# Optimization experiments

Measured on AMD Instinct MI355X. Metric: run time of the kernel, lower is better.

The kernel has to match this reference:

```python
import jax, jax.numpy as jnp
import numpy as np

D = 1024       # hidden_size
H = 16         # num_heads
DH = D // H    # d_keys = d_values = 64
FF = int(D * 2.0)  # mlp hidden
EPS = 1e-6


def _ln(t):
    # LayerNorm, elementwise_affine=False
    mu = jnp.mean(t, axis=-1, keepdims=True)
    var = jnp.mean((t - mu) ** 2, axis=-1, keepdims=True)
    return (t - mu) * jax.lax.rsqrt(var + EPS)


def setup_inputs() -> dict:
    key = jax.random.key(0)
    ks = jax.random.split(key, 16)
    B, L = 2, 2048
    s = 0.02
    return {
        "x": jax.random.normal(ks[0], (B, L, D), jnp.float32),
        "c": jax.random.normal(ks[1], (B, 1, D), jnp.float32),
        "Wq": jax.random.normal(ks[2], (D, D), jnp.float32) * s,
        "bq": jnp.zeros((D,), jnp.float32),
        "Wk": jax.random.normal(ks[3], (D, D), jnp.float32) * s,
        "bk": jnp.zeros((D,), jnp.float32),
        "Wv": jax.random.normal(ks[4], (D, D), jnp.float32) * s,
        "bv": jnp.zeros((D,), jnp.float32),
        "Wo": jax.random.normal(ks[5], (D, D), jnp.float32) * s,
        "bo": jnp.zeros((D,), jnp.float32),
        "W1": jax.random.normal(ks[6], (D, FF), jnp.float32) * s,
        "b1": jnp.zeros((FF,), jnp.float32),
        "W2": jax.random.normal(ks[7], (FF, D), jnp.float32) * s,
        "b2": jnp.zeros((D,), jnp.float32),
        "Wada": jax.random.normal(ks[8], (D, 6 * D), jnp.float32) * s,
        "bada": jnp.zeros((6 * D,), jnp.float32),
    }


def reference(x, c, Wq, bq, Wk, bk, Wv, bv, Wo, bo, W1, b1, W2, b2, Wada, bada):
    B, L, _ = x.shape
    # adaLN-Zero modulation params (dropout layers act as identity in eval)
    ada = jax.nn.silu(c) @ Wada + bada  # [B,1,6D]
    shift_msa, scale_msa, gate_msa, shift_mlp, scale_mlp, gate_mlp = jnp.split(ada, 6, axis=-1)

    # --- attention branch ---
    h = _ln(x) * (1.0 + scale_msa) + shift_msa
    q = (h @ Wq + bq).reshape(B, L, H, DH)
    k = (h @ Wk + bk).reshape(B, L, H, DH)
    v = (h @ Wv + bv).reshape(B, L, H, DH)
    scale = 1.0 / np.sqrt(DH).astype(np.float32)
    scores = jnp.einsum('blhe,bshe->bhls', q, k)  # full LxL scores, as in source
    A = jax.nn.softmax(scale * scores, axis=-1)
    out = jnp.einsum('bhls,bshd->blhd', A, v)     # [B,L,H,DH]
    # mix=True: transpose(2,1) then view(B,L,-1) -> head/position mixing reshape
    out = jnp.transpose(out, (0, 2, 1, 3)).reshape(B, L, H * DH)
    x = x + gate_msa * (out @ Wo + bo)

    # --- MLP branch (exact GELU: nn.GELU() passed as act_layer) ---
    h2 = _ln(x) * (1.0 + scale_mlp) + shift_mlp
    m = jax.nn.gelu(h2 @ W1 + b1, approximate=False) @ W2 + b2
    return x + gate_mlp * m
```

## Files before the change

### kernel.cpp

```cpp
#include <hip/hip_runtime.h>
#include <hip/hip_bf16.h>

typedef unsigned short ushort_t;
typedef __bf16 bf16x8 __attribute__((ext_vector_type(8)));
typedef float f32x4 __attribute__((ext_vector_type(4)));

typedef unsigned int u32;
typedef u32 __attribute__((address_space(1))) global_u32;
typedef u32 __attribute__((address_space(3))) lds_u32;

#define D_ 1024
#define L_ 2048
#define B_ 2
#define H_ 16
#define DH_ 64
#define FF_ 2048
#define ADA_ 6144
#define BHL_ (B_ * H_ * L_)

#define MFMA __builtin_amdgcn_mfma_f32_16x16x32_bf16

__device__ __forceinline__ ushort_t f2bf(float f) {
    union { float f; u32 u; } v; v.f = f;
    u32 r = v.u + 0x7fffu + ((v.u >> 16) & 1u);
    return (ushort_t)(r >> 16);
}

__device__ __forceinline__ u32 pk_bf16(float a, float b) {
    float2 f; f.x = a; f.y = b;
    __hip_bfloat162 t = __float22bfloat162_rn(f);
    union { __hip_bfloat162 b2; u32 u; } v; v.b2 = t; return v.u;
}

__device__ __forceinline__ void llds16(const ushort_t* src, ushort_t* dst) {
    __builtin_amdgcn_global_load_lds((global_u32*)src, (lds_u32*)dst, 16, 0, 0);
}

__global__ void transpose_w_all(
    const float* __restrict__ Wq, const float* __restrict__ Wk,
    const float* __restrict__ Wv, const float* __restrict__ Wo,
    const float* __restrict__ W1, const float* __restrict__ W2,
    ushort_t* __restrict__ Wqkv, ushort_t* __restrict__ Wo_t,
    ushort_t* __restrict__ W1_t, ushort_t* __restrict__ W2_t) {
    __shared__ float tile[64][65];
    int id = blockIdx.x;
    const float* W; ushort_t* Wt; int K, N, ntx, lid;
    if (id < 1024) {
        int which = id >> 8; lid = id & 255; K = 1024; N = 1024; ntx = 16;
        W  = which == 0 ? Wq : which == 1 ? Wk : which == 2 ? Wv : Wo;
        Wt = which == 3 ? Wo_t : Wqkv + (size_t)which * 1024 * 1024;
    } else if (id < 1536) {
        lid = id - 1024; W = W1; Wt = W1_t; K = 1024; N = 2048; ntx = 32;
    } else {
        lid = id - 1536; W = W2; Wt = W2_t; K = 2048; N = 1024; ntx = 16;
    }
    int n0 = (lid % ntx) * 64, k0 = (lid / ntx) * 64;
    int t = threadIdx.x;
    for (int p = 0; p < 4; ++p) {
        int k = p * 16 + (t >> 4), nn = (t & 15) * 4;
        float4 v = *(const float4*)(W + (size_t)(k0 + k) * N + n0 + nn);
        tile[k][nn] = v.x; tile[k][nn + 1] = v.y; tile[k][nn + 2] = v.z; tile[k][nn + 3] = v.w;
    }
    __syncthreads();
    for (int p = 0; p < 4; ++p) {
        int n = p * 16 + (t >> 4), kk = (t & 15) * 4;
        ushort4 o;
        o.x = f2bf(tile[kk][n]); o.y = f2bf(tile[kk + 1][n]);
        o.z = f2bf(tile[kk + 2][n]); o.w = f2bf(tile[kk + 3][n]);
        *(ushort4*)(Wt + (size_t)(n0 + n) * K + k0 + kk) = o;
    }
}

__global__ void transpose_v(const ushort_t* __restrict__ V, ushort_t* __restrict__ Vt) {
    __shared__ ushort_t tile[64][72];
    int bh = blockIdx.y, l0 = blockIdx.x * 64;
    const ushort_t* Vb = V + ((size_t)bh * L_ + l0) * DH_;
    ushort_t* Vtb = Vt + (size_t)bh * DH_ * L_;
    int t = threadIdx.x;
    for (int p = 0; p < 2; ++p) {
        int i = p * 32 + (t >> 3), d0 = (t & 7) * 8;
        ushort4 v0 = *(const ushort4*)(Vb + (size_t)i * DH_ + d0);
        ushort4 v1 = *(const ushort4*)(Vb + (size_t)i * DH_ + d0 + 4);
        tile[d0 + 0][i] = v0.x; tile[d0 + 1][i] = v0.y; tile[d0 + 2][i] = v0.z; tile[d0 + 3][i] = v0.w;
        tile[d0 + 4][i] = v1.x; tile[d0 + 5][i] = v1.y; tile[d0 + 6][i] = v1.z; tile[d0 + 7][i] = v1.w;
    }
    __syncthreads();
    for (int p = 0; p < 2; ++p) {
        int dh = p * 32 + (t >> 3), j0 = (t & 7) * 8;
        ushort4 o0, o1;
        o0.x = tile[dh][j0 + 0]; o0.y = tile[dh][j0 + 1]; o0.z = tile[dh][j0 + 2]; o0.w = tile[dh][j0 + 3];
        o1.x = tile[dh][j0 + 4]; o1.y = tile[dh][j0 + 5]; o1.z = tile[dh][j0 + 6]; o1.w = tile[dh][j0 + 7];
        *(ushort4*)(Vtb + (size_t)dh * L_ + l0 + j0) = o0;
        *(ushort4*)(Vtb + (size_t)dh * L_ + l0 + j0 + 4) = o1;
    }
}

__global__ void ada_gemv(const float* __restrict__ c, const float* __restrict__ Wada,
                         float* __restrict__ partial) {
    int ks = blockIdx.y;
    int j = blockIdx.x * 256 + threadIdx.x;
    __shared__ float s0[64], s1[64];
    if (threadIdx.x < 64) {
        float v = c[ks * 64 + threadIdx.x];
        s0[threadIdx.x] = v / (1.f + __expf(-v));
        v = c[D_ + ks * 64 + threadIdx.x];
        s1[threadIdx.x] = v / (1.f + __expf(-v));
    }
    __syncthreads();
    float a0 = 0.f, a1 = 0.f;
#pragma unroll 8
    for (int d = 0; d < 64; ++d) {
        float w = Wada[(size_t)(ks * 64 + d) * ADA_ + j];
        a0 = fmaf(s0[d], w, a0);
        a1 = fmaf(s1[d], w, a1);
    }
    partial[(size_t)(ks * 2 + 0) * ADA_ + j] = a0;
    partial[(size_t)(ks * 2 + 1) * ADA_ + j] = a1;
}

__global__ void ada_reduce(const float* __restrict__ partial,
                           const float* __restrict__ bada, float* __restrict__ ada) {
    int j = blockIdx.x * 256 + threadIdx.x;
    float a0 = bada[j], a1 = bada[j];
#pragma unroll
    for (int ks = 0; ks < 16; ++ks) {
        a0 += partial[(size_t)(ks * 2 + 0) * ADA_ + j];
        a1 += partial[(size_t)(ks * 2 + 1) * ADA_ + j];
    }
    ada[j] = a0;
    ada[ADA_ + j] = a1;
}

__global__ void ln_mod(const float* __restrict__ x, const float* __restrict__ ada,
                       int so, int co, ushort_t* __restrict__ out) {
    int row = blockIdx.x;
    int b = row >> 11;
    float4 v = ((const float4*)(x + (size_t)row * D_))[threadIdx.x];
    float sum = v.x + v.y + v.z + v.w;
    float sq = v.x * v.x + v.y * v.y + v.z * v.z + v.w * v.w;
    for (int off = 32; off; off >>= 1) { sum += __shfl_down(sum, off); sq += __shfl_down(sq, off); }
    __shared__ float sa[4], sb[4];
    int wave = threadIdx.x >> 6, lane = threadIdx.x & 63;
    if (lane == 0) { sa[wave] = sum; sb[wave] = sq; }
    __syncthreads();
    sum = sa[0] + sa[1] + sa[2] + sa[3];
    sq = sb[0] + sb[1] + sb[2] + sb[3];
    float mean = sum * (1.f / 1024.f);
    float var = sq * (1.f / 1024.f) - mean * mean;
    float rstd = rsqrtf(var + 1e-6f);
    int d = threadIdx.x * 4;
    const float* shf = ada + (size_t)b * ADA_ + so;
    const float* scf = ada + (size_t)b * ADA_ + co;
    uint2 ov;
    ov.x = pk_bf16((v.x - mean) * rstd * (1.f + scf[d + 0]) + shf[d + 0],
                   (v.y - mean) * rstd * (1.f + scf[d + 1]) + shf[d + 1]);
    ov.y = pk_bf16((v.z - mean) * rstd * (1.f + scf[d + 2]) + shf[d + 2],
                   (v.w - mean) * rstd * (1.f + scf[d + 3]) + shf[d + 3]);
    *(uint2*)(out + (size_t)row * D_ + d) = ov;
}

struct EpiArgs {
    const float* bias0; const float* bias1; const float* bias2;
    ushort_t* o0; ushort_t* o1; ushort_t* o2;
    const float* resid; const float* gate;
    float* fout;
};

template <int EPI>
__device__ __forceinline__ void epi_store(float v, int m, int n, int N, const EpiArgs& e) {
    if (EPI == 0) {
        int which = n >> 10, cc = n & 1023;
        const float* bias = which == 0 ? e.bias0 : which == 1 ? e.bias1 : e.bias2;
        ushort_t* ob = which == 0 ? e.o0 : which == 1 ? e.o1 : e.o2;
        v += bias[cc];
        if (which == 0) v *= 0.18033688f;
        int b = m >> 11, l = m & 2047, h = cc >> 6, dh = cc & 63;
        ob[(((size_t)(b * H_ + h) * L_) + l) * DH_ + dh] = f2bf(v);
    } else if (EPI == 1) {
        v += e.bias0[n];
        v = 0.5f * v * (1.f + erff(v * 0.70710678118f));
        e.o0[(size_t)m * N + n] = f2bf(v);
    } else {
        int b = m >> 11;
        e.fout[(size_t)m * N + n] =
            e.resid[(size_t)m * N + n] + e.gate[(size_t)b * ADA_ + n] * (v + e.bias0[n]);
    }
}

template <int EPI>
__device__ __forceinline__ void st4(const f32x4& cc, int mb, int n, int N, const EpiArgs& e) {
#pragma unroll
    for (int r = 0; r < 4; ++r) epi_store<EPI>(cc[r], mb + r, n, N, e);
}

template <int EPI>
__global__ __launch_bounds__(256, 2) void gemm_bt(
    const ushort_t* __restrict__ A, const ushort_t* __restrict__ Bt,
    int M, int N, int K, EpiArgs e) {
    __shared__ ushort_t As[128 * 64];
    __shared__ ushort_t Bs[128 * 64];
    int m0 = blockIdx.x * 128, n0 = blockIdx.y * 128;
    int tid = threadIdx.x, wave = tid >> 6, lane = tid & 63;
    int quad = lane >> 4, lc = lane & 15;
    int wm = (wave & 1) * 64, wn = (wave >> 1) * 64;
    int srow = lane >> 3, sg = lane & 7;
    int sw = lc & 7;

    const ushort_t* stp[8];
    ushort_t* stl[8];
#pragma unroll
    for (int i = 0; i < 8; ++i) {
        int chunk = wave * 8 + i;
        int c = chunk & 15;
        int row = c * 8 + srow;
        stp[i] = (chunk < 16 ? A + (size_t)(m0 + row) * K
                             : Bt + (size_t)(n0 + row) * K) + (sg ^ srow) * 8;
        stl[i] = (chunk < 16 ? As : Bs) + c * 512 + lane * 8;
    }

    f32x4 c00 = {}, c01 = {}, c02 = {}, c03 = {};
    f32x4 c10 = {}, c11 = {}, c12 = {}, c13 = {};
    f32x4 c20 = {}, c21 = {}, c22 = {}, c23 = {};
    f32x4 c30 = {}, c31 = {}, c32 = {}, c33 = {};

    for (int k0 = 0; k0 < K; k0 += 64) {
#pragma unroll
        for (int i = 0; i < 8; ++i) { llds16(stp[i], stl[i]); stp[i] += 64; }
        __syncthreads();
#pragma unroll
        for (int kk = 0; kk < 2; ++kk) {
            int off = ((kk * 4 + quad) ^ sw) * 8;
            bf16x8 a0 = *(const bf16x8*)&As[(wm +  0 + lc) * 64 + off];
            bf16x8 a1 = *(const bf16x8*)&As[(wm + 16 + lc) * 64 + off];
            bf16x8 a2 = *(const bf16x8*)&As[(wm + 32 + lc) * 64 + off];
            bf16x8 a3 = *(const bf16x8*)&As[(wm + 48 + lc) * 64 + off];
            bf16x8 b0 = *(const bf16x8*)&Bs[(wn +  0 + lc) * 64 + off];
            bf16x8 b1 = *(const bf16x8*)&Bs[(wn + 16 + lc) * 64 + off];
            bf16x8 b2 = *(const bf16x8*)&Bs[(wn + 32 + lc) * 64 + off];
            bf16x8 b3 = *(const bf16x8*)&Bs[(wn + 48 + lc) * 64 + off];
            c00 = MFMA(a0, b0, c00, 0, 0, 0); c01 = MFMA(a0, b1, c01, 0, 0, 0);
            c02 = MFMA(a0, b2, c02, 0, 0, 0); c03 = MFMA(a0, b3, c03, 0, 0, 0);
            c10 = MFMA(a1, b0, c10, 0, 0, 0); c11 = MFMA(a1, b1, c11, 0, 0, 0);
            c12 = MFMA(a1, b2, c12, 0, 0, 0); c13 = MFMA(a1, b3, c13, 0, 0, 0);
            c20 = MFMA(a2, b0, c20, 0, 0, 0); c21 = MFMA(a2, b1, c21, 0, 0, 0);
            c22 = MFMA(a2, b2, c22, 0, 0, 0); c23 = MFMA(a2, b3, c23, 0, 0, 0);
            c30 = MFMA(a3, b0, c30, 0, 0, 0); c31 = MFMA(a3, b1, c31, 0, 0, 0);
            c32 = MFMA(a3, b2, c32, 0, 0, 0); c33 = MFMA(a3, b3, c33, 0, 0, 0);
        }
        __syncthreads();
    }

    int mb = m0 + wm + quad * 4, nb = n0 + wn + lc;
    st4<EPI>(c00, mb +  0, nb +  0, N, e); st4<EPI>(c01, mb +  0, nb + 16, N, e);
    st4<EPI>(c02, mb +  0, nb + 32, N, e); st4<EPI>(c03, mb +  0, nb + 48, N, e);
    st4<EPI>(c10, mb + 16, nb +  0, N, e); st4<EPI>(c11, mb + 16, nb + 16, N, e);
    st4<EPI>(c12, mb + 16, nb + 32, N, e); st4<EPI>(c13, mb + 16, nb + 48, N, e);
    st4<EPI>(c20, mb + 32, nb +  0, N, e); st4<EPI>(c21, mb + 32, nb + 16, N, e);
    st4<EPI>(c22, mb + 32, nb + 32, N, e); st4<EPI>(c23, mb + 32, nb + 48, N, e);
    st4<EPI>(c30, mb + 48, nb +  0, N, e); st4<EPI>(c31, mb + 48, nb + 16, N, e);
    st4<EPI>(c32, mb + 48, nb + 32, N, e); st4<EPI>(c33, mb + 48, nb + 48, N, e);
}

template <int EPI>
__global__ __launch_bounds__(256, 2) void gemm_bt64(
    const ushort_t* __restrict__ A, const ushort_t* __restrict__ Bt,
    int M, int N, int K, EpiArgs e) {
    __shared__ ushort_t As[64 * 64];
    __shared__ ushort_t Bs[128 * 64];
    int m0 = blockIdx.x * 64, n0 = blockIdx.y * 128;
    int tid = threadIdx.x, wave = tid >> 6, lane = tid & 63;
    int quad = lane >> 4, lc = lane & 15;
    int wn = wave * 32;
    int srow = lane >> 3, sg = lane & 7;
    int sw = lc & 7;

    const ushort_t* stp[6];
    ushort_t* stl[6];
#pragma unroll
    for (int i = 0; i < 6; ++i) {
        int chunk = wave * 6 + i;
        if (chunk < 8) {
            int row = chunk * 8 + srow;
            stp[i] = A + (size_t)(m0 + row) * K + (sg ^ srow) * 8;
            stl[i] = &As[chunk * 512 + lane * 8];
        } else {
            int c = chunk - 8;
            int row = c * 8 + srow;
            stp[i] = Bt + (size_t)(n0 + row) * K + (sg ^ srow) * 8;
            stl[i] = &Bs[c * 512 + lane * 8];
        }
    }

    f32x4 c00 = {}, c01 = {};
    f32x4 c10 = {}, c11 = {};
    f32x4 c20 = {}, c21 = {};
    f32x4 c30 = {}, c31 = {};

    for (int k0 = 0; k0 < K; k0 += 64) {
#pragma unroll
        for (int i = 0; i < 6; ++i) { llds16(stp[i], stl[i]); stp[i] += 64; }
        __syncthreads();
#pragma unroll
        for (int kk = 0; kk < 2; ++kk) {
            int off = ((kk * 4 + quad) ^ sw) * 8;
            bf16x8 a0 = *(const bf16x8*)&As[( 0 + lc) * 64 + off];
            bf16x8 a1 = *(const bf16x8*)&As[(16 + lc) * 64 + off];
            bf16x8 a2 = *(const bf16x8*)&As[(32 + lc) * 64 + off];
            bf16x8 a3 = *(const bf16x8*)&As[(48 + lc) * 64 + off];
            bf16x8 b0 = *(const bf16x8*)&Bs[(wn +  0 + lc) * 64 + off];
            bf16x8 b1 = *(const bf16x8*)&Bs[(wn + 16 + lc) * 64 + off];
            c00 = MFMA(a0, b0, c00, 0, 0, 0); c01 = MFMA(a0, b1, c01, 0, 0, 0);
            c10 = MFMA(a1, b0, c10, 0, 0, 0); c11 = MFMA(a1, b1, c11, 0, 0, 0);
            c20 = MFMA(a2, b0, c20, 0, 0, 0); c21 = MFMA(a2, b1, c21, 0, 0, 0);
            c30 = MFMA(a3, b0, c30, 0, 0, 0); c31 = MFMA(a3, b1, c31, 0, 0, 0);
        }
        __syncthreads();
    }

    int mb = m0 + quad * 4, nb = n0 + wn + lc;
    st4<EPI>(c00, mb +  0, nb + 0, N, e); st4<EPI>(c01, mb +  0, nb + 16, N, e);
    st4<EPI>(c10, mb + 16, nb + 0, N, e); st4<EPI>(c11, mb + 16, nb + 16, N, e);
    st4<EPI>(c20, mb + 32, nb + 0, N, e); st4<EPI>(c21, mb + 32, nb + 16, N, e);
    st4<EPI>(c30, mb + 48, nb + 0, N, e); st4<EPI>(c31, mb + 48, nb + 16, N, e);
}

__global__ __launch_bounds__(256, 2) void attn(
    const ushort_t* __restrict__ Q, const ushort_t* __restrict__ Kx,
    const ushort_t* __restrict__ Vt,
    ushort_t* __restrict__ Op0, ushort_t* __restrict__ Op1,
    ushort_t* __restrict__ Op2, ushort_t* __restrict__ Op3,
    float* __restrict__ lsum) {
    __shared__ ushort_t Ks[128 * 64];
    __shared__ ushort_t Vs[64 * 128];
    __shared__ ushort_t Ps[4 * 16 * 128];
    int id = blockIdx.x;
    int bh = ((id & 7) << 2) + ((id >> 3) & 3);
    int quarter = (id >> 5) & 3;
    int qt = id >> 7;
    const ushort_t* Qg = Q + ((size_t)bh * L_ + qt * 128) * DH_;
    const ushort_t* Kg = Kx + (size_t)bh * L_ * DH_;
    const ushort_t* Vg = Vt + (size_t)bh * DH_ * L_;
    int tid = threadIdx.x, wave = tid >> 6, lane = tid & 63;
    int quad = lane >> 4, lc = lane & 15;
    int sw = lc & 7;
    int srow = lane >> 3, sg = lane & 7;

    const ushort_t* stp[8];
    ushort_t* stl[8];
    int stinc;
    if (wave < 2) {
        stinc = 128 * DH_;
#pragma unroll
        for (int i = 0; i < 8; ++i) {
            int chunk = wave * 8 + i;
            int row = chunk * 8 + srow;
            stp[i] = Kg + (size_t)(quarter * 512 + row) * DH_ + (sg ^ srow) * 8;
            stl[i] = &Ks[chunk * 512 + lane * 8];
        }
    } else {
        stinc = 128;
#pragma unroll
        for (int i = 0; i < 8; ++i) {
            int c2 = (wave - 2) * 8 + i;
            int row = c2 * 4 + (lane >> 4);
            int g = (lane & 15) ^ (row & 15);
            stp[i] = Vg + (size_t)row * L_ + quarter * 512 + g * 8;
            stl[i] = &Vs[c2 * 512 + lane * 8];
        }
    }

    const ushort_t* qp = Qg + (size_t)(wave * 32 + lc) * DH_ + quad * 8;
    bf16x8 q00 = *(const bf16x8*)(qp);
    bf16x8 q01 = *(const bf16x8*)(qp + 32);
    bf16x8 q10 = *(const bf16x8*)(qp + 16 * DH_);
    bf16x8 q11 = *(const bf16x8*)(qp + 16 * DH_ + 32);

    f32x4 o00 = {}, o01 = {}, o02 = {}, o03 = {};
    f32x4 o10 = {}, o11 = {}, o12 = {}, o13 = {};
    float lrow0 = 0.f, lrow1 = 0.f;
    ushort_t* Pw = &Ps[wave * 16 * 128];

    for (int t = 0; t < 4; ++t) {
#pragma unroll
        for (int i = 0; i < 8; ++i) { llds16(stp[i], stl[i]); stp[i] += stinc; }
        __syncthreads();

        f32x4 s[2][8];
#pragma unroll
        for (int kk = 0; kk < 2; ++kk) {
            int off = ((kk * 4 + quad) ^ sw) * 8;
            bf16x8 aq0 = kk == 0 ? q00 : q01;
            bf16x8 aq1 = kk == 0 ? q10 : q11;
#pragma unroll
            for (int ni = 0; ni < 8; ++ni) {
                bf16x8 bk = *(const bf16x8*)&Ks[(ni * 16 + lc) * 64 + off];
                if (kk == 0) {
                    f32x4 z = {0.f, 0.f, 0.f, 0.f};
                    s[0][ni] = MFMA(bk, aq0, z, 0, 0, 0);
                    s[1][ni] = MFMA(bk, aq1, z, 0, 0, 0);
                } else {
                    s[0][ni] = MFMA(bk, aq0, s[0][ni], 0, 0, 0);
                    s[1][ni] = MFMA(bk, aq1, s[1][ni], 0, 0, 0);
                }
            }
        }

#pragma unroll
        for (int pi = 0; pi < 2; ++pi) {
            float acc = 0.f;
#pragma unroll
            for (int ni = 0; ni < 8; ++ni) {
                float p0 = __builtin_amdgcn_exp2f(s[pi][ni][0]);
                float p1 = __builtin_amdgcn_exp2f(s[pi][ni][1]);
                float p2 = __builtin_amdgcn_exp2f(s[pi][ni][2]);
                float p3 = __builtin_amdgcn_exp2f(s[pi][ni][3]);
                acc += (p0 + p1) + (p2 + p3);
                uint2 pk; pk.x = pk_bf16(p0, p1); pk.y = pk_bf16(p2, p3);
                int cg = ni * 2 + (quad >> 1);
                *(uint2*)&Pw[lc * 128 + ((cg ^ lc) & 15) * 8 + (quad & 1) * 4] = pk;
            }
            acc += __shfl_xor(acc, 16);
            acc += __shfl_xor(acc, 32);
            if (pi == 0) lrow0 += acc; else lrow1 += acc;

#pragma unroll
            for (int kk = 0; kk < 4; ++kk) {
                int gq = kk * 4 + quad;
                bf16x8 ap  = *(const bf16x8*)&Pw[lc * 128 + ((gq ^ lc) & 15) * 8];
                bf16x8 bv0 = *(const bf16x8*)&Vs[( 0 + lc) * 128 + ((gq ^ lc) * 8)];
                bf16x8 bv1 = *(const bf16x8*)&Vs[(16 + lc) * 128 + ((gq ^ lc) * 8)];
                bf16x8 bv2 = *(const bf16x8*)&Vs[(32 + lc) * 128 + ((gq ^ lc) * 8)];
                bf16x8 bv3 = *(const bf16x8*)&Vs[(48 + lc) * 128 + ((gq ^ lc) * 8)];
                if (pi == 0) {
                    o00 = MFMA(ap, bv0, o00, 0, 0, 0); o01 = MFMA(ap, bv1, o01, 0, 0, 0);
                    o02 = MFMA(ap, bv2, o02, 0, 0, 0); o03 = MFMA(ap, bv3, o03, 0, 0, 0);
                } else {
                    o10 = MFMA(ap, bv0, o10, 0, 0, 0); o11 = MFMA(ap, bv1, o11, 0, 0, 0);
                    o12 = MFMA(ap, bv2, o12, 0, 0, 0); o13 = MFMA(ap, bv3, o13, 0, 0, 0);
                }
            }
        }
        __syncthreads();
    }

    ushort_t* Op = quarter == 0 ? Op0 : quarter == 1 ? Op1 : quarter == 2 ? Op2 : Op3;
#pragma unroll
    for (int pi = 0; pi < 2; ++pi) {
#pragma unroll
        for (int nio = 0; nio < 4; ++nio) {
            const f32x4& ov = pi == 0 ? (nio == 0 ? o00 : nio == 1 ? o01 : nio == 2 ? o02 : o03)
                                      : (nio == 0 ? o10 : nio == 1 ? o11 : nio == 2 ? o12 : o13);
#pragma unroll
            for (int r = 0; r < 4; ++r) {
                int row = qt * 128 + wave * 32 + pi * 16 + quad * 4 + r;
                Op[((size_t)bh * L_ + row) * DH_ + nio * 16 + lc] = f2bf(ov[r]);
            }
        }
    }
    if (quad == 0) {
        int base = qt * 128 + wave * 32;
        lsum[(size_t)quarter * BHL_ + (size_t)bh * L_ + base + lc] = lrow0;
        lsum[(size_t)quarter * BHL_ + (size_t)bh * L_ + base + 16 + lc] = lrow1;
    }
}

__global__ void attn_merge(const ushort_t* __restrict__ Op0,
                           const ushort_t* __restrict__ Op1,
                           const ushort_t* __restrict__ Op2,
                           const ushort_t* __restrict__ Op3,
                           const float* __restrict__ lsum,
                           ushort_t* __restrict__ O) {
    int gid = blockIdx.x * 256 + threadIdx.x;
    int row = gid >> 3, j = gid & 7;
    float inv = 1.f / (lsum[row] + lsum[BHL_ + row] +
                       lsum[2 * BHL_ + row] + lsum[3 * BHL_ + row]);
    bf16x8 v0 = *(const bf16x8*)(Op0 + (size_t)row * DH_ + j * 8);
    bf16x8 v1 = *(const bf16x8*)(Op1 + (size_t)row * DH_ + j * 8);
    bf16x8 v2 = *(const bf16x8*)(Op2 + (size_t)row * DH_ + j * 8);
    bf16x8 v3 = *(const bf16x8*)(Op3 + (size_t)row * DH_ + j * 8);
    uint4 o;
    float r0, r1;
#pragma unroll
    for (int k = 0; k < 4; ++k) {
        r0 = ((float)v0[2 * k] + (float)v1[2 * k] + (float)v2[2 * k] + (float)v3[2 * k]) * inv;
        r1 = ((float)v0[2 * k + 1] + (float)v1[2 * k + 1] + (float)v2[2 * k + 1] + (float)v3[2 * k + 1]) * inv;
        ((u32*)&o)[k] = pk_bf16(r0, r1);
    }
    *(uint4*)(O + (size_t)row * DH_ + j * 8) = o;
}

extern "C" void kernel_launch(void* const* d_in, const int* in_sizes, int n_in,
                              void* d_out, int out_size, void* d_ws, size_t ws_size,
                              hipStream_t stream) {
    (void)in_sizes; (void)n_in; (void)out_size; (void)ws_size;
    const float* x    = (const float*)d_in[0];
    const float* c    = (const float*)d_in[1];
    const float* Wq   = (const float*)d_in[2];
    const float* bq   = (const float*)d_in[3];
    const float* Wk   = (const float*)d_in[4];
    const float* bk   = (const float*)d_in[5];
    const float* Wv   = (const float*)d_in[6];
    const float* bv   = (const float*)d_in[7];
    const float* Wo   = (const float*)d_in[8];
    const float* bo   = (const float*)d_in[9];
    const float* W1   = (const float*)d_in[10];
    const float* b1   = (const float*)d_in[11];
    const float* W2   = (const float*)d_in[12];
    const float* b2   = (const float*)d_in[13];
    const float* Wada = (const float*)d_in[14];
    const float* bada = (const float*)d_in[15];

    char* w = (char*)d_ws;
    float*    ada  = (float*)(w + 0);
    ushort_t* Wqkv = (ushort_t*)(w + 49152);
    ushort_t* Wo_t = (ushort_t*)(w + 6340608);
    ushort_t* W1_t = (ushort_t*)(w + 8437760);
    ushort_t* W2_t = (ushort_t*)(w + 12632064);
    ushort_t* h    = (ushort_t*)(w + 16826368);
    ushort_t* Qb   = (ushort_t*)(w + 25214976);
    ushort_t* Kb   = (ushort_t*)(w + 33603584);
    ushort_t* Vb   = (ushort_t*)(w + 41992192);
    ushort_t* Vtb  = (ushort_t*)(w + 50380800);
    float*    x1   = (float*)(w + 58769408);
    ushort_t* Ob   = Qb;
    ushort_t* m1   = Qb;
    float*    lsb  = (float*)Wqkv;
    float*    adap = (float*)Vtb;
    ushort_t* p2   = (ushort_t*)x1;
    ushort_t* p3   = (ushort_t*)((char*)x1 + 8388608);

    const int M = B_ * L_;

    transpose_w_all<<<2048, 256, 0, stream>>>(Wq, Wk, Wv, Wo, W1, W2,
                                              Wqkv, Wo_t, W1_t, W2_t);

    ada_gemv<<<dim3(24, 16), 256, 0, stream>>>(c, Wada, adap);
    ada_reduce<<<24, 256, 0, stream>>>(adap, bada, ada);
    ln_mod<<<M, 256, 0, stream>>>(x, ada, 0, 1024, h);

    EpiArgs e0 = {bq, bk, bv, Qb, Kb, Vb, nullptr, nullptr, nullptr};
    gemm_bt<0><<<dim3(32, 24), 256, 0, stream>>>(h, Wqkv, M, 3072, D_, e0);

    transpose_v<<<dim3(32, 32), 256, 0, stream>>>(Vb, Vtb);

    attn<<<2048, 256, 0, stream>>>(Qb, Kb, Vtb, Vb, h, p2, p3, lsb);
    attn_merge<<<2048, 256, 0, stream>>>(Vb, h, p2, p3, lsb, Ob);

    EpiArgs e1 = {bo, nullptr, nullptr, nullptr, nullptr, nullptr, x, ada + 2048, x1};
    gemm_bt64<2><<<dim3(64, 8), 256, 0, stream>>>(Ob, Wo_t, M, D_, D_, e1);

    ln_mod<<<M, 256, 0, stream>>>(x1, ada, 3072, 4096, h);

    EpiArgs e2 = {b1, nullptr, nullptr, m1, nullptr, nullptr, nullptr, nullptr, nullptr};
    gemm_bt64<1><<<dim3(64, 16), 256, 0, stream>>>(h, W1_t, M, FF_, D_, e2);

    EpiArgs e3 = {b2, nullptr, nullptr, nullptr, nullptr, nullptr, x1, ada + 5120, (float*)d_out};
    gemm_bt64<2><<<dim3(64, 8), 256, 0, stream>>>(m1, W2_t, M, D_, FF_, e3);
}
```

Baseline: 323.6 us.

## Double-buffer K/V tiles in attention kernel and raise MFMA wave priority

Double-buffers the K and V shared-memory tiles in the attention kernel. The next tile is issued with direct global-to-LDS loads before the current tile is computed, and partial vmcnt waits plus raw barriers hide global latency behind the MFMA work. It also raises wave priority around the MFMA sections with s_setprio. The extra 32 KB of LDS per block may cut occupancy below the requested two blocks per CU, and the hand-written waitcnt counts must match the number of loads in flight.

```diff
diff --git a/kernel.cpp b/kernel.cpp
--- a/kernel.cpp
+++ b/kernel.cpp
@@ -330,8 +330,8 @@
     ushort_t* __restrict__ Op0, ushort_t* __restrict__ Op1,
     ushort_t* __restrict__ Op2, ushort_t* __restrict__ Op3,
     float* __restrict__ lsum) {
-    __shared__ ushort_t Ks[128 * 64];
-    __shared__ ushort_t Vs[64 * 128];
+    __shared__ ushort_t Ks[2][128 * 64];
+    __shared__ ushort_t Vs[2][64 * 128];
     __shared__ ushort_t Ps[4 * 16 * 128];
     int id = blockIdx.x;
     int bh = ((id & 7) << 2) + ((id >> 3) & 3);
@@ -355,7 +355,7 @@
             int chunk = wave * 8 + i;
             int row = chunk * 8 + srow;
             stp[i] = Kg + (size_t)(quarter * 512 + row) * DH_ + (sg ^ srow) * 8;
-            stl[i] = &Ks[chunk * 512 + lane * 8];
+            stl[i] = &Ks[0][chunk * 512 + lane * 8];
         }
     } else {
         stinc = 128;
@@ -365,9 +365,12 @@
             int row = c2 * 4 + (lane >> 4);
             int g = (lane & 15) ^ (row & 15);
             stp[i] = Vg + (size_t)row * L_ + quarter * 512 + g * 8;
-            stl[i] = &Vs[c2 * 512 + lane * 8];
-        }
-    }
+            stl[i] = &Vs[0][c2 * 512 + lane * 8];
+        }
+    }
+
+#pragma unroll
+    for (int i = 0; i < 8; ++i) { llds16(stp[i], stl[i]); stp[i] += stinc; }
 
     const ushort_t* qp = Qg + (size_t)(wave * 32 + lc) * DH_ + quad * 8;
     bf16x8 q00 = *(const bf16x8*)(qp);
@@ -381,11 +384,21 @@
     ushort_t* Pw = &Ps[wave * 16 * 128];
 
     for (int t = 0; t < 4; ++t) {
-#pragma unroll
-        for (int i = 0; i < 8; ++i) { llds16(stp[i], stl[i]); stp[i] += stinc; }
-        __syncthreads();
+        if (t < 3) {
+            int nbuf = (t + 1) & 1;
+#pragma unroll
+            for (int i = 0; i < 8; ++i) { llds16(stp[i], stl[i] + nbuf * 8192); stp[i] += stinc; }
+            asm volatile("s_waitcnt vmcnt(8)" ::: "memory");
+        } else {
+            asm volatile("s_waitcnt vmcnt(0)" ::: "memory");
+        }
+        __builtin_amdgcn_s_barrier();
+        asm volatile("" ::: "memory");
+        const ushort_t* Ksb = &Ks[t & 1][0];
+        const ushort_t* Vsb = &Vs[t & 1][0];
 
         f32x4 s[2][8];
+        __builtin_amdgcn_s_setprio(1);
 #pragma unroll
         for (int kk = 0; kk < 2; ++kk) {
             int off = ((kk * 4 + quad) ^ sw) * 8;
@@ -393,7 +406,7 @@
             bf16x8 aq1 = kk == 0 ? q10 : q11;
 #pragma unroll
             for (int ni = 0; ni < 8; ++ni) {
-                bf16x8 bk = *(const bf16x8*)&Ks[(ni * 16 + lc) * 64 + off];
+                bf16x8 bk = *(const bf16x8*)&Ksb[(ni * 16 + lc) * 64 + off];
                 if (kk == 0) {
                     f32x4 z = {0.f, 0.f, 0.f, 0.f};
                     s[0][ni] = MFMA(bk, aq0, z, 0, 0, 0);
@@ -404,6 +417,7 @@
                 }
             }
         }
+        __builtin_amdgcn_s_setprio(0);
 
 #pragma unroll
         for (int pi = 0; pi < 2; ++pi) {
@@ -423,14 +437,15 @@
             acc += __shfl_xor(acc, 32);
             if (pi == 0) lrow0 += acc; else lrow1 += acc;
 
+            __builtin_amdgcn_s_setprio(1);
 #pragma unroll
             for (int kk = 0; kk < 4; ++kk) {
                 int gq = kk * 4 + quad;
                 bf16x8 ap  = *(const bf16x8*)&Pw[lc * 128 + ((gq ^ lc) & 15) * 8];
-                bf16x8 bv0 = *(const bf16x8*)&Vs[( 0 + lc) * 128 + ((gq ^ lc) * 8)];
-                bf16x8 bv1 = *(const bf16x8*)&Vs[(16 + lc) * 128 + ((gq ^ lc) * 8)];
-                bf16x8 bv2 = *(const bf16x8*)&Vs[(32 + lc) * 128 + ((gq ^ lc) * 8)];
-                bf16x8 bv3 = *(const bf16x8*)&Vs[(48 + lc) * 128 + ((gq ^ lc) * 8)];
+                bf16x8 bv0 = *(const bf16x8*)&Vsb[( 0 + lc) * 128 + ((gq ^ lc) * 8)];
+                bf16x8 bv1 = *(const bf16x8*)&Vsb[(16 + lc) * 128 + ((gq ^ lc) * 8)];
+                bf16x8 bv2 = *(const bf16x8*)&Vsb[(32 + lc) * 128 + ((gq ^ lc) * 8)];
+                bf16x8 bv3 = *(const bf16x8*)&Vsb[(48 + lc) * 128 + ((gq ^ lc) * 8)];
                 if (pi == 0) {
                     o00 = MFMA(ap, bv0, o00, 0, 0, 0); o01 = MFMA(ap, bv1, o01, 0, 0, 0);
                     o02 = MFMA(ap, bv2, o02, 0, 0, 0); o03 = MFMA(ap, bv3, o03, 0, 0, 0);
@@ -439,8 +454,10 @@
                     o12 = MFMA(ap, bv2, o12, 0, 0, 0); o13 = MFMA(ap, bv3, o13, 0, 0, 0);
                 }
             }
-        }
-        __syncthreads();
+            __builtin_amdgcn_s_setprio(0);
+        }
+        asm volatile("" ::: "memory");
+        __builtin_amdgcn_s_barrier();
     }
 
     ushort_t* Op = quarter == 0 ? Op0 : quarter == 1 ? Op1 : quarter == 2 ? Op2 : Op3;
```

Measured after the change: 339.0 us. 4.8% more time.

## Keep softmax probabilities in registers by permuting K rows to match MFMA layout

Applied to the files above, without the earlier changes.

Stops staging the bf16 probability tile through shared memory between the QK and PV MFMAs. K rows are loaded in a permuted order so the QK accumulator layout already matches the A-operand layout the PV MFMA needs, and packed probabilities are assembled directly into MFMA operands. This removes LDS writes and reads plus 16 KB of shared memory per block. In exchange it holds more live registers (the px/py arrays), which could limit occupancy.

```diff
diff --git a/kernel.cpp b/kernel.cpp
--- a/kernel.cpp
+++ b/kernel.cpp
@@ -332,7 +332,6 @@
     float* __restrict__ lsum) {
     __shared__ ushort_t Ks[128 * 64];
     __shared__ ushort_t Vs[64 * 128];
-    __shared__ ushort_t Ps[4 * 16 * 128];
     int id = blockIdx.x;
     int bh = ((id & 7) << 2) + ((id >> 3) & 3);
     int quarter = (id >> 5) & 3;
@@ -353,8 +352,10 @@
 #pragma unroll
         for (int i = 0; i < 8; ++i) {
             int chunk = wave * 8 + i;
-            int row = chunk * 8 + srow;
-            stp[i] = Kg + (size_t)(quarter * 512 + row) * DH_ + (sg ^ srow) * 8;
+            int slot = chunk * 8 + srow;
+            int s5 = slot & 31;
+            int sig = (slot & ~31) + ((s5 & 15) >> 2) * 8 + (s5 & 3) + (s5 >> 4) * 4;
+            stp[i] = Kg + (size_t)(quarter * 512 + sig) * DH_ + (sg ^ srow) * 8;
             stl[i] = &Ks[chunk * 512 + lane * 8];
         }
     } else {
@@ -378,7 +379,6 @@
     f32x4 o00 = {}, o01 = {}, o02 = {}, o03 = {};
     f32x4 o10 = {}, o11 = {}, o12 = {}, o13 = {};
     float lrow0 = 0.f, lrow1 = 0.f;
-    ushort_t* Pw = &Ps[wave * 16 * 128];
 
     for (int t = 0; t < 4; ++t) {
 #pragma unroll
@@ -405,6 +405,7 @@
             }
         }
 
+        u32 px[2][8], py[2][8];
 #pragma unroll
         for (int pi = 0; pi < 2; ++pi) {
             float acc = 0.f;
@@ -415,30 +416,30 @@
                 float p2 = __builtin_amdgcn_exp2f(s[pi][ni][2]);
                 float p3 = __builtin_amdgcn_exp2f(s[pi][ni][3]);
                 acc += (p0 + p1) + (p2 + p3);
-                uint2 pk; pk.x = pk_bf16(p0, p1); pk.y = pk_bf16(p2, p3);
-                int cg = ni * 2 + (quad >> 1);
-                *(uint2*)&Pw[lc * 128 + ((cg ^ lc) & 15) * 8 + (quad & 1) * 4] = pk;
+                px[pi][ni] = pk_bf16(p0, p1);
+                py[pi][ni] = pk_bf16(p2, p3);
             }
             acc += __shfl_xor(acc, 16);
             acc += __shfl_xor(acc, 32);
             if (pi == 0) lrow0 += acc; else lrow1 += acc;
-
-#pragma unroll
-            for (int kk = 0; kk < 4; ++kk) {
-                int gq = kk * 4 + quad;
-                bf16x8 ap  = *(const bf16x8*)&Pw[lc * 128 + ((gq ^ lc) & 15) * 8];
-                bf16x8 bv0 = *(const bf16x8*)&Vs[( 0 + lc) * 128 + ((gq ^ lc) * 8)];
-                bf16x8 bv1 = *(const bf16x8*)&Vs[(16 + lc) * 128 + ((gq ^ lc) * 8)];
-                bf16x8 bv2 = *(const bf16x8*)&Vs[(32 + lc) * 128 + ((gq ^ lc) * 8)];
-                bf16x8 bv3 = *(const bf16x8*)&Vs[(48 + lc) * 128 + ((gq ^ lc) * 8)];
-                if (pi == 0) {
-                    o00 = MFMA(ap, bv0, o00, 0, 0, 0); o01 = MFMA(ap, bv1, o01, 0, 0, 0);
-                    o02 = MFMA(ap, bv2, o02, 0, 0, 0); o03 = MFMA(ap, bv3, o03, 0, 0, 0);
-                } else {
-                    o10 = MFMA(ap, bv0, o10, 0, 0, 0); o11 = MFMA(ap, bv1, o11, 0, 0, 0);
-                    o12 = MFMA(ap, bv2, o12, 0, 0, 0); o13 = MFMA(ap, bv3, o13, 0, 0, 0);
-                }
-            }
+        }
+
+#pragma unroll
+        for (int kk = 0; kk < 4; ++kk) {
+            int gq = kk * 4 + quad;
+            bf16x8 bv0 = *(const bf16x8*)&Vs[( 0 + lc) * 128 + ((gq ^ lc) * 8)];
+            bf16x8 bv1 = *(const bf16x8*)&Vs[(16 + lc) * 128 + ((gq ^ lc) * 8)];
+            bf16x8 bv2 = *(const bf16x8*)&Vs[(32 + lc) * 128 + ((gq ^ lc) * 8)];
+            bf16x8 bv3 = *(const bf16x8*)&Vs[(48 + lc) * 128 + ((gq ^ lc) * 8)];
+            union { u32 u[4]; bf16x8 v; } a0, a1;
+            a0.u[0] = px[0][2 * kk]; a0.u[1] = py[0][2 * kk];
+            a0.u[2] = px[0][2 * kk + 1]; a0.u[3] = py[0][2 * kk + 1];
+            a1.u[0] = px[1][2 * kk]; a1.u[1] = py[1][2 * kk];
+            a1.u[2] = px[1][2 * kk + 1]; a1.u[3] = py[1][2 * kk + 1];
+            o00 = MFMA(a0.v, bv0, o00, 0, 0, 0); o01 = MFMA(a0.v, bv1, o01, 0, 0, 0);
+            o02 = MFMA(a0.v, bv2, o02, 0, 0, 0); o03 = MFMA(a0.v, bv3, o03, 0, 0, 0);
+            o10 = MFMA(a1.v, bv0, o10, 0, 0, 0); o11 = MFMA(a1.v, bv1, o11, 0, 0, 0);
+            o12 = MFMA(a1.v, bv2, o12, 0, 0, 0); o13 = MFMA(a1.v, bv3, o13, 0, 0, 0);
         }
         __syncthreads();
     }
```

Result: no change. 324.3 us (+0.2%).
